# Kernel tuning notes

Measured on AMD Instinct MI355X. Metric: run time of the kernel, lower is better.

Reference implementation:

```python
import jax, jax.numpy as jnp
import numpy as np
from jax import lax

HID = 256
ITERS = 8
KT, KH, KW = 3, 7, 7
NBLK = 3
B_, T_, H_, W_, CIN = 1, 8, 32, 32, 128
NQ = 256


def _layernorm(x, scale, bias, eps=1e-6):
    mu = jnp.mean(x, axis=-1, keepdims=True)
    var = jnp.mean(jnp.square(x - mu), axis=-1, keepdims=True)
    return (x - mu) * lax.rsqrt(var + eps) * scale + bias


def _convssm3d(x, A_kernel, B_kernel):
    # x: (B,T,H,W,C); kernels: (C,kt,kh,kw)
    B, T, H, W, C = x.shape
    A_stable = 0.9 * jnp.tanh(A_kernel)
    tt = (jnp.arange(KT) - KT // 2) % T
    th = (jnp.arange(KH) - KH // 2) % H
    tw = (jnp.arange(KW) - KW // 2) % W
    TT, TH, TW = jnp.meshgrid(tt, th, tw, indexing='ij')

    def to_freq(k):
        pad = jnp.zeros((C, T, H, W), x.dtype).at[:, TT, TH, TW].set(k)
        return jnp.fft.fftn(pad, axes=(1, 2, 3)).transpose(1, 2, 3, 0)[None]  # (1,T,H,W,C)

    A_f = to_freq(A_stable)
    B_f = to_freq(B_kernel)
    Bx_f = B_f * jnp.fft.fftn(x, axes=(1, 2, 3))
    shape = (ITERS,) + x.shape
    a_seq = jnp.broadcast_to(A_f, shape)
    b_seq = jnp.broadcast_to(Bx_f, shape)

    def op(left, right):
        return (left[0] * right[0], right[0] * left[1] + right[1])

    _, h_all = lax.associative_scan(op, (a_seq, b_seq), axis=0)
    return jnp.fft.ifftn(h_all[-1], axes=(1, 2, 3)).real


def setup_inputs() -> dict:
    key = jax.random.key(0)
    ks = jax.random.split(key, 10)
    s = 0.02
    return {
        'video_features': jax.random.normal(ks[0], (B_, T_, H_, W_, CIN), jnp.float32),
        'query_points': jax.random.uniform(ks[1], (B_, NQ, 3), jnp.float32),
        'conv_w': jax.random.normal(ks[2], (CIN, HID), jnp.float32) * s,
        'conv_b': jnp.zeros((HID,), jnp.float32),
        'A_kernels': jax.random.normal(ks[3], (NBLK, HID, KT, KH, KW), jnp.float32) * s,
        'B_kernels': jax.random.normal(ks[4], (NBLK, HID, KT, KH, KW), jnp.float32) * s,
        'ln_scale': jnp.ones((NBLK, HID), jnp.float32),
        'ln_bias': jnp.zeros((NBLK, HID), jnp.float32),
        'mlp_w1': jax.random.normal(ks[5], (NBLK, HID, 4 * HID), jnp.float32) * s,
        'mlp_b1': jnp.zeros((NBLK, 4 * HID), jnp.float32),
        'mlp_w2': jax.random.normal(ks[6], (NBLK, 4 * HID, HID), jnp.float32) * s,
        'mlp_b2': jnp.zeros((NBLK, HID), jnp.float32),
        'traj_w': jax.random.normal(ks[7], (HID, 2), jnp.float32) * s,
        'traj_b': jnp.zeros((2,), jnp.float32),
        'occ_w': jax.random.normal(ks[8], (HID, 1), jnp.float32) * s,
        'occ_b': jnp.zeros((1,), jnp.float32),
    }


def reference(video_features, query_points, conv_w, conv_b, A_kernels, B_kernels,
              ln_scale, ln_bias, mlp_w1, mlp_b1, mlp_w2, mlp_b2,
              traj_w, traj_b, occ_w, occ_b):
    # 1x1x1 conv == channel dense. Query scatter in original is a zeros no-op.
    x = jnp.einsum('bthwc,cd->bthwd', video_features, conv_w) + conv_b
    for i in range(NBLK):
        h = _convssm3d(x, A_kernels[i], B_kernels[i])
        h = _layernorm(h, ln_scale[i], ln_bias[i])
        x = x + h
        m = jax.nn.gelu(x @ mlp_w1[i] + mlp_b1[i])  # approximate gelu (flax default)
        x = x + (m @ mlp_w2[i] + mlp_b2[i])
    feat = jnp.mean(x, axis=(2, 3))  # (B,T,C)
    N = query_points.shape[1]
    fe = jnp.broadcast_to(feat[:, None], (feat.shape[0], N) + feat.shape[1:])  # (B,N,T,C)
    trajectories = fe @ traj_w + traj_b + query_points[..., 1:3][:, :, None, :]  # (B,N,T,2)
    occlusion = jax.nn.sigmoid((fe @ occ_w + occ_b)[..., 0])  # (B,N,T)
    return trajectories, occlusion
```

## Files before the change

### kernel.cpp

```cpp
#include <hip/hip_runtime.h>
#include <hip/hip_bf16.h>
#include <math.h>

#define Tn 8
#define Hn 32
#define Wn 32
#define Pn 8192
#define Cn 256
#define CINn 128
#define NTAP 147
#define PADW 40

typedef short s8v __attribute__((ext_vector_type(8)));
typedef float f4v __attribute__((ext_vector_type(4)));
typedef __hip_bfloat16 bf16;

__device__ __forceinline__ float gelu_f(float v) {
    return 0.5f * v * (1.0f + tanhf(0.7978845608028654f * (v + 0.044715f * v * v * v)));
}

__device__ __forceinline__ void gload_lds16(const bf16* g, bf16* l) {
    __builtin_amdgcn_global_load_lds(
        (const __attribute__((address_space(1))) void*)g,
        (__attribute__((address_space(3))) void*)l, 16, 0, 0);
}

__device__ __forceinline__ size_t caddrA(int K, int m, int k) {
    return ((size_t)(m >> 7) * (K >> 6) + (k >> 6)) * 8192 +
           (size_t)((((k >> 3) & 7) * 128 + (m & 127)) * 8 + (k & 7));
}
__device__ __forceinline__ size_t caddrB(int K, int BN, int n, int k) {
    return ((size_t)(n / BN) * (K >> 6) + (k >> 6)) * (size_t)(BN * 64) +
           (size_t)((((k >> 3) & 7) * BN + (n % BN)) * 8 + (k & 7));
}

__global__ __launch_bounds__(256) void tcast_all_k(
        const float* __restrict__ convw, const float* __restrict__ w1,
        const float* __restrict__ w2, const float* __restrict__ video,
        bf16* __restrict__ cwT, bf16* __restrict__ w1T, bf16* __restrict__ w2T,
        bf16* __restrict__ vb) {
    const int z = blockIdx.z;
    const int tid = (int)threadIdx.x;
    if (z == 7) {
        const int bx = (int)blockIdx.y * 32 + (int)blockIdx.x;
        const int i = bx * 256 + tid;
        const int p = i >> 5, c0 = (i & 31) * 4;
        const float4 v = ((const float4*)video)[i];
        const size_t a0 = caddrA(CINn, p, c0);
        vb[a0 + 0] = __float2bfloat16(v.x);
        vb[a0 + 1] = __float2bfloat16(v.y);
        vb[a0 + 2] = __float2bfloat16(v.z);
        vb[a0 + 3] = __float2bfloat16(v.w);
        return;
    }
    const float* in;
    bf16* out;
    int R, C, bn;
    if (z == 0)      { in = convw;                       out = cwT;                          R = CINn; C = Cn;   bn = 32; }
    else if (z < 4)  { const int i = z - 1;
                       in = w1 + (size_t)i * Cn * 1024;  out = w1T + (size_t)i * 1024 * Cn;  R = Cn;   C = 1024; bn = 64; }
    else             { const int i = z - 4;
                       in = w2 + (size_t)i * 1024 * Cn;  out = w2T + (size_t)i * Cn * 1024;  R = 1024; C = Cn;   bn = 32; }
    if ((int)blockIdx.x >= (C >> 5) || (int)blockIdx.y >= (R >> 5)) return;

    __shared__ float tile[32][33];
    const int tx = tid & 31, ty = tid >> 5;
    const int rb = blockIdx.y << 5, cb = blockIdx.x << 5;
#pragma unroll
    for (int p = 0; p < 4; ++p)
        tile[ty + p * 8][tx] = in[(size_t)(rb + ty + p * 8) * C + cb + tx];
    __syncthreads();
#pragma unroll
    for (int p = 0; p < 4; ++p)
        out[caddrB(R, bn, cb + ty + p * 8, rb + tx)] = __float2bfloat16(tile[tx][ty + p * 8]);
}

template <int BN, int MODE, int ACH>
__global__ __launch_bounds__(256) void gemm_bf16_k(
        const bf16* __restrict__ A, const bf16* __restrict__ Wt,
        const float* __restrict__ bias, float* __restrict__ Cf,
        bf16* __restrict__ Cb, bf16* __restrict__ Cpl, int M, int N, int K) {
    constexpr int BM = 128;
    constexpr int NW = BN / 2;
    constexpr int NF = BN / 32;
    constexpr int ALOADS = 4;
    constexpr int BLOADS = (BN * 8) / 256;
    __shared__ s8v As[8 * BM];
    __shared__ s8v Bs[8 * BN];

    const int tid = (int)threadIdx.x;
    const int lane = tid & 63, wid = tid >> 6;
    const int wm = wid & 1, wn = wid >> 1;
    const int l15 = lane & 15, l4 = lane >> 4;
    const int m0 = blockIdx.y * BM;
    const int n0 = blockIdx.x * BN;

    f4v acc[4][NF];
#pragma unroll
    for (int i = 0; i < 4; ++i)
#pragma unroll
        for (int j = 0; j < NF; ++j)
#pragma unroll
            for (int r = 0; r < 4; ++r) acc[i][j][r] = 0.f;

    const bf16* Ach = A + ((size_t)(m0 >> 7) * (K >> 6)) * 8192;
    const bf16* Aln[ALOADS];
    if (ACH == 0) {
#pragma unroll
        for (int j = 0; j < ALOADS; ++j) {
            const int cid = j * 256 + tid;
            Aln[j] = A + (size_t)(m0 + (cid & (BM - 1))) * K + (cid / BM) * 8;
        }
    }
    const bf16* Bch = Wt + ((size_t)(n0 / BN) * (K >> 6)) * (size_t)(BN * 64);

    int kc = 0;
    for (int kb = 0; kb < K; kb += 64, ++kc) {
        if (ACH == 1) {
#pragma unroll
            for (int j = 0; j < ALOADS; ++j)
                gload_lds16(Ach + (size_t)kc * 8192 + (j * 256 + tid) * 8,
                            (bf16*)&As[j * 256 + tid]);
        } else {
#pragma unroll
            for (int j = 0; j < ALOADS; ++j)
                gload_lds16(Aln[j] + kb, (bf16*)&As[j * 256 + tid]);
        }
#pragma unroll
        for (int j = 0; j < BLOADS; ++j)
            gload_lds16(Bch + (size_t)kc * (BN * 64) + (j * 256 + tid) * 8,
                        (bf16*)&Bs[j * 256 + tid]);
        __syncthreads();

        s8v af[2][4], bfr[2][NF];
#pragma unroll
        for (int ks = 0; ks < 2; ++ks) {
#pragma unroll
            for (int i = 0; i < 4; ++i)
                af[ks][i] = As[(ks * 4 + l4) * BM + wm * 64 + i * 16 + l15];
#pragma unroll
            for (int j = 0; j < NF; ++j)
                bfr[ks][j] = Bs[(ks * 4 + l4) * BN + wn * NW + j * 16 + l15];
        }
#pragma unroll
        for (int ks = 0; ks < 2; ++ks)
#pragma unroll
            for (int i = 0; i < 4; ++i)
#pragma unroll
                for (int j = 0; j < NF; ++j)
                    acc[i][j] = __builtin_amdgcn_mfma_f32_16x16x32_bf16(
                        af[ks][i], bfr[ks][j], acc[i][j], 0, 0, 0);
        __syncthreads();
    }

#pragma unroll
    for (int i = 0; i < 4; ++i) {
        const int rbase = m0 + wm * 64 + i * 16 + l4 * 4;
#pragma unroll
        for (int j = 0; j < NF; ++j) {
            const int col = n0 + wn * NW + j * 16 + l15;
            const float bv = bias[col];
#pragma unroll
            for (int r = 0; r < 4; ++r) {
                const size_t idx = (size_t)(rbase + r) * N + col;
                float v = acc[i][j][r] + bv;
                if (MODE == 0) Cf[idx] = v;
                if (MODE == 1) Cb[caddrA(N, rbase + r, col)] = __float2bfloat16(gelu_f(v));
                if (MODE == 2) { v += Cf[idx]; Cf[idx] = v; }
                if (MODE != 1 && Cpl != nullptr)
                    Cpl[(size_t)col * Pn + rbase + r] = __float2bfloat16(v);
            }
        }
    }
}

#define CLOADS(AS, BS0, BS1, body) do {                                       \
    const int bb_ = (body);                                                   \
    const int kt_ = bb_ < 7 ? 0 : (bb_ < 14 ? 1 : 2);                         \
    const int kh_ = bb_ - kt_ * 7;                                            \
    BS0 = *(const s8v*)&tw[bb_][u0][0];                                       \
    BS1 = *(const s8v*)&tw[bb_][u1][0];                                       \
    _Pragma("unroll")                                                         \
    for (int i_ = 0; i_ < 2; ++i_) {                                          \
        const int tp_ = (tout[i_] - kt_ + 9) & 7;                             \
        const int hin_ = (hl[i_] + 35 - kh_) & 31;                            \
        AS[i_] = *(const s8v*)&pl[(tp_ * 32 + hin_) * PADW + aoff];           \
    }                                                                         \
} while (0)

#define CMFMA(AS, BS0, BS1) do {                                              \
    _Pragma("unroll")                                                         \
    for (int i_ = 0; i_ < 2; ++i_) {                                          \
        acc[i_][0] = __builtin_amdgcn_mfma_f32_16x16x32_bf16(AS[i_], BS0, acc[i_][0], 0, 0, 0); \
        acc[i_][1] = __builtin_amdgcn_mfma_f32_16x16x32_bf16(AS[i_], BS1, acc[i_][1], 0, 0, 0); \
    }                                                                         \
} while (0)

__global__ __launch_bounds__(512) void conv_ssm_k(
        const bf16* __restrict__ xplb,
        const float* __restrict__ Ak,
        const float* __restrict__ Bk,
        float* __restrict__ hpo) {
    __shared__ __align__(16) bf16 Pl[2][256 * PADW];
    __shared__ __align__(16) bf16 Tw[2][21][32][8];
    __shared__ float wtap[2][NTAP];

    const int c = blockIdx.x;
    const int tid = (int)threadIdx.x;
    const int lane = tid & 63, wv = tid >> 6;
    const int l15 = lane & 15, l4 = lane >> 4;

    if (tid < NTAP) {
        wtap[0][tid] = Bk[(size_t)c * NTAP + tid];
        wtap[1][tid] = 0.9f * tanhf(Ak[(size_t)c * NTAP + tid]);
    }
    {
        const s8v* src = (const s8v*)(xplb + (size_t)c * Pn);
#pragma unroll
        for (int j = 0; j < 2; ++j) {
            const int g = j * 512 + tid;
            *(s8v*)&Pl[0][(g >> 2) * PADW + (g & 3) * 8] = src[g];
        }
    }
    __syncthreads();
    for (int e = tid; e < 2 * 21 * 32; e += 512) {
        const int sel = e / 672, rem = e % 672;
        const int body = rem >> 5, u = rem & 31;
        const float* tp = &wtap[sel][body * 7];
        bf16 row[8];
#pragma unroll
        for (int j = 0; j < 8; ++j) {
            const int kw = (u - j) & 31;
            row[j] = __float2bfloat16((kw < 7) ? tp[kw] : 0.f);
        }
        *(s8v*)&Tw[sel][body][u][0] = *(const s8v*)row;
    }

    const int u0 = (l15 - l4 * 8 + 3) & 31;
    const int u1 = (l15 + 16 - l4 * 8 + 3) & 31;
    int tout[2], hl[2];
#pragma unroll
    for (int i = 0; i < 2; ++i) {
        const int f = wv * 2 + i;
        tout[i] = f >> 1;
        hl[i] = ((f & 1) << 4) + l15;
    }
    const int aoff = l4 * 8;

    float hsum[16];
#pragma unroll
    for (int i = 0; i < 16; ++i) hsum[i] = 0.f;
    __syncthreads();

#pragma unroll 1
    for (int it = 0; it < 8; ++it) {
        const bf16* pl = Pl[it & 1];
        bf16* pd = Pl[(it + 1) & 1];
        const bf16 (*tw)[32][8] = Tw[(it == 0) ? 0 : 1];

        f4v acc[2][2];
#pragma unroll
        for (int i = 0; i < 2; ++i)
#pragma unroll
            for (int hf = 0; hf < 2; ++hf)
#pragma unroll
                for (int r = 0; r < 4; ++r) acc[i][hf][r] = 0.f;

        s8v a0[2], a1[2], b00, b01, b10, b11;
        CLOADS(a0, b00, b01, 0);
#pragma unroll 1
        for (int b = 0; b < 20; b += 2) {
            CLOADS(a1, b10, b11, b + 1);
            CMFMA(a0, b00, b01);
            CLOADS(a0, b00, b01, b + 2);
            CMFMA(a1, b10, b11);
        }
        CMFMA(a0, b00, b01);

#pragma unroll
        for (int i = 0; i < 2; ++i) {
            const int rbase = (wv * 2 + i) * 16 + l4 * 4;
#pragma unroll
            for (int hf = 0; hf < 2; ++hf) {
                const int col = l15 + hf * 16;
#pragma unroll
                for (int r = 0; r < 4; ++r) {
                    const float v = acc[i][hf][r];
                    hsum[i * 8 + hf * 4 + r] += v;
                    if (it < 7) pd[(rbase + r) * PADW + col] = __float2bfloat16(v);
                }
            }
        }
        __syncthreads();
    }

    float* o = hpo + (size_t)c * Pn;
#pragma unroll
    for (int i = 0; i < 2; ++i) {
        const int rbase = (wv * 2 + i) * 16 + l4 * 4;
#pragma unroll
        for (int hf = 0; hf < 2; ++hf)
#pragma unroll
            for (int r = 0; r < 4; ++r)
                o[(rbase + r) * 32 + l15 + hf * 16] = hsum[i * 8 + hf * 4 + r];
    }
}

__global__ __launch_bounds__(256) void ln_res_plane_k(
        const float* __restrict__ hpl,
        const float* __restrict__ scale, const float* __restrict__ bias,
        float* __restrict__ x,
        bf16* __restrict__ xb) {
    __shared__ float tile[256][33];
    __shared__ float red[2][32][9];
    __shared__ float mus[32], rss[32];
    const int tid = (int)threadIdx.x;
    const int p0 = blockIdx.x << 5;

    {
        const float* src = hpl + (size_t)tid * Pn + p0;
#pragma unroll
        for (int j = 0; j < 32; j += 4) {
            const float4 v = *(const float4*)(src + j);
            tile[tid][j] = v.x; tile[tid][j + 1] = v.y;
            tile[tid][j + 2] = v.z; tile[tid][j + 3] = v.w;
        }
    }
    __syncthreads();
    {
        const int p = tid & 31, g = tid >> 5;
        float s = 0.f, ss = 0.f;
#pragma unroll
        for (int ci = 0; ci < 32; ++ci) {
            const float v = tile[g * 32 + ci][p];
            s += v; ss += v * v;
        }
        red[0][p][g] = s; red[1][p][g] = ss;
    }
    __syncthreads();
    if (tid < 32) {
        float s = 0.f, ss = 0.f;
#pragma unroll
        for (int g = 0; g < 8; ++g) { s += red[0][tid][g]; ss += red[1][tid][g]; }
        const float mu = s * (1.0f / 256.0f);
        const float var = ss * (1.0f / 256.0f) - mu * mu;
        mus[tid] = mu;
        rss[tid] = rsqrtf(var + 1e-6f);
    }
    __syncthreads();
    {
        const int cch = tid;
        const float sc = scale[cch], bi = bias[cch];
#pragma unroll 4
        for (int j = 0; j < 32; ++j) {
            const size_t idx = (size_t)(p0 + j) * Cn + cch;
            const float normed = (tile[cch][j] - mus[j]) * rss[j] * sc + bi;
            const float xv = x[idx] + normed;
            x[idx] = xv;
            xb[idx] = __float2bfloat16(xv);
        }
    }
}

__global__ void feat_part_k(const float* __restrict__ x, float* __restrict__ part) {
    const int t = blockIdx.x, sgm = blockIdx.y;
    const int c = (int)threadIdx.x;
    float acc = 0.f;
    const float* xp_ = x + ((size_t)t * 1024 + sgm * 128) * Cn + c;
    for (int p = 0; p < 128; ++p) acc += xp_[(size_t)p * Cn];
    part[(t * 8 + sgm) * Cn + c] = acc;
}

__global__ __launch_bounds__(256) void heads_k(
        const float* __restrict__ part, const float* __restrict__ qp,
        const float* __restrict__ traj_w, const float* __restrict__ traj_b,
        const float* __restrict__ occ_w, const float* __restrict__ occ_b,
        float* __restrict__ out) {
    __shared__ float fs[Tn * Cn];
    __shared__ float proj[Tn][3];
    const int tid = (int)threadIdx.x;
    for (int i = tid; i < Tn * Cn; i += 256) {
        const int t = i >> 8, c = i & 255;
        float s = 0.f;
#pragma unroll
        for (int j = 0; j < 8; ++j) s += part[(t * 8 + j) * Cn + c];
        fs[i] = s * (1.0f / 1024.0f);
    }
    __syncthreads();
    if (tid < 24) {
        const int t = tid / 3, j = tid % 3;
        float s = 0.f;
        for (int c = 0; c < Cn; ++c) {
            const float w = (j < 2) ? traj_w[c * 2 + j] : occ_w[c];
            s += fs[t * Cn + c] * w;
        }
        s += (j < 2) ? traj_b[j] : occ_b[0];
        proj[t][j] = s;
    }
    __syncthreads();
    const int n = tid;
#pragma unroll
    for (int t = 0; t < Tn; ++t) {
        out[(n * Tn + t) * 2 + 0] = proj[t][0] + qp[n * 3 + 1];
        out[(n * Tn + t) * 2 + 1] = proj[t][1] + qp[n * 3 + 2];
        out[4096 + n * Tn + t] = 1.0f / (1.0f + expf(-proj[t][2]));
    }
}

extern "C" void kernel_launch(void* const* d_in, const int* in_sizes, int n_in,
                              void* d_out, int out_size, void* d_ws, size_t ws_size,
                              hipStream_t stream) {
    const float* video = (const float*)d_in[0];
    const float* qp    = (const float*)d_in[1];
    const float* convw = (const float*)d_in[2];
    const float* convb = (const float*)d_in[3];
    const float* Ak    = (const float*)d_in[4];
    const float* Bk    = (const float*)d_in[5];
    const float* ln_s  = (const float*)d_in[6];
    const float* ln_b  = (const float*)d_in[7];
    const float* w1    = (const float*)d_in[8];
    const float* b1    = (const float*)d_in[9];
    const float* w2    = (const float*)d_in[10];
    const float* b2    = (const float*)d_in[11];
    const float* tw    = (const float*)d_in[12];
    const float* tb    = (const float*)d_in[13];
    const float* ow    = (const float*)d_in[14];
    const float* ob    = (const float*)d_in[15];

    char* wsb = (char*)d_ws;
    float* x    = (float*)wsb;           wsb += (size_t)Pn * Cn * 4;
    float* hpl  = (float*)wsb;           wsb += (size_t)Pn * Cn * 4;
    bf16*  xplb = (bf16*)wsb;            wsb += (size_t)Pn * Cn * 2;
    bf16*  xb   = (bf16*)wsb;            wsb += (size_t)Pn * Cn * 2;
    bf16*  mb   = (bf16*)wsb;            wsb += (size_t)Pn * 1024 * 2;
    bf16*  vb   = (bf16*)wsb;            wsb += (size_t)Pn * CINn * 2;
    bf16*  cwT  = (bf16*)wsb;            wsb += (size_t)Cn * CINn * 2;
    bf16*  w1T  = (bf16*)wsb;            wsb += (size_t)3 * 1024 * Cn * 2;
    bf16*  w2T  = (bf16*)wsb;            wsb += (size_t)3 * Cn * 1024 * 2;
    float* part = (float*)wsb;           wsb += (size_t)64 * Cn * 4;

    tcast_all_k<<<dim3(32, 32, 8), 256, 0, stream>>>(convw, w1, w2, video,
                                                     cwT, w1T, w2T, vb);

    gemm_bf16_k<32, 0, 1><<<dim3(Cn / 32, Pn / 128), 256, 0, stream>>>(
        vb, cwT, convb, x, nullptr, xplb, Pn, Cn, CINn);

    for (int i = 0; i < 3; ++i) {
        conv_ssm_k<<<Cn, 512, 0, stream>>>(xplb, Ak + (size_t)i * Cn * NTAP,
                                           Bk + (size_t)i * Cn * NTAP, hpl);
        ln_res_plane_k<<<Pn / 32, 256, 0, stream>>>(hpl, ln_s + i * Cn,
                                                    ln_b + i * Cn, x, xb);
        gemm_bf16_k<64, 1, 0><<<dim3(1024 / 64, Pn / 128), 256, 0, stream>>>(
            xb, w1T + (size_t)i * 1024 * Cn, b1 + (size_t)i * 1024, nullptr, mb,
            nullptr, Pn, 1024, Cn);
        gemm_bf16_k<32, 2, 1><<<dim3(Cn / 32, Pn / 128), 256, 0, stream>>>(
            mb, w2T + (size_t)i * Cn * 1024, b2 + (size_t)i * Cn, x, nullptr,
            (i < 2) ? xplb : nullptr, Pn, Cn, 1024);
    }

    feat_part_k<<<dim3(Tn, 8), 256, 0, stream>>>(x, part);
    heads_k<<<1, 256, 0, stream>>>(part, qp, tw, tb, ow, ob, (float*)d_out);
}
```

Measured before the change: 293.8 us.

## Double GEMM K-step per barrier and store SSM output in bf16

The GEMM kernel now loads two 64-wide K chunks into doubled LDS buffers before each barrier pair, which halves the number of __syncthreads per K loop. Separately, the conv-SSM output plane is written as bf16 instead of fp32, and the layernorm kernel reads bf16 and converts it back to float. This halves that intermediate's memory traffic. The cost is twice the LDS per GEMM block, which may lower occupancy, and bf16 rounding of the SSM output before layernorm.

```diff
diff --git a/kernel.cpp b/kernel.cpp
--- a/kernel.cpp
+++ b/kernel.cpp
@@ -17,6 +17,9 @@
 
 __device__ __forceinline__ float gelu_f(float v) {
     return 0.5f * v * (1.0f + tanhf(0.7978845608028654f * (v + 0.044715f * v * v * v)));
+}
+__device__ __forceinline__ float bf2f(short s) {
+    return __uint_as_float(((unsigned)(unsigned short)s) << 16);
 }
 
 __device__ __forceinline__ void gload_lds16(const bf16* g, bf16* l) {
@@ -83,10 +86,9 @@
     constexpr int BM = 128;
     constexpr int NW = BN / 2;
     constexpr int NF = BN / 32;
-    constexpr int ALOADS = 4;
     constexpr int BLOADS = (BN * 8) / 256;
-    __shared__ s8v As[8 * BM];
-    __shared__ s8v Bs[8 * BN];
+    __shared__ s8v As[16 * BM];
+    __shared__ s8v Bs[16 * BN];
 
     const int tid = (int)threadIdx.x;
     const int lane = tid & 63, wid = tid >> 6;
@@ -104,52 +106,55 @@
             for (int r = 0; r < 4; ++r) acc[i][j][r] = 0.f;
 
     const bf16* Ach = A + ((size_t)(m0 >> 7) * (K >> 6)) * 8192;
-    const bf16* Aln[ALOADS];
+    const bf16* Aln[4];
     if (ACH == 0) {
 #pragma unroll
-        for (int j = 0; j < ALOADS; ++j) {
+        for (int j = 0; j < 4; ++j) {
             const int cid = j * 256 + tid;
             Aln[j] = A + (size_t)(m0 + (cid & (BM - 1))) * K + (cid / BM) * 8;
         }
     }
     const bf16* Bch = Wt + ((size_t)(n0 / BN) * (K >> 6)) * (size_t)(BN * 64);
 
-    int kc = 0;
-    for (int kb = 0; kb < K; kb += 64, ++kc) {
-        if (ACH == 1) {
-#pragma unroll
-            for (int j = 0; j < ALOADS; ++j)
-                gload_lds16(Ach + (size_t)kc * 8192 + (j * 256 + tid) * 8,
-                            (bf16*)&As[j * 256 + tid]);
-        } else {
-#pragma unroll
-            for (int j = 0; j < ALOADS; ++j)
-                gload_lds16(Aln[j] + kb, (bf16*)&As[j * 256 + tid]);
-        }
-#pragma unroll
-        for (int j = 0; j < BLOADS; ++j)
-            gload_lds16(Bch + (size_t)kc * (BN * 64) + (j * 256 + tid) * 8,
-                        (bf16*)&Bs[j * 256 + tid]);
+    for (int kb = 0; kb < K; kb += 128) {
+        const int kc = kb >> 6;
+#pragma unroll
+        for (int u = 0; u < 2; ++u) {
+            if (ACH == 1) {
+#pragma unroll
+                for (int j = 0; j < 4; ++j)
+                    gload_lds16(Ach + (size_t)(kc + u) * 8192 + (j * 256 + tid) * 8,
+                                (bf16*)&As[u * 1024 + j * 256 + tid]);
+            } else {
+#pragma unroll
+                for (int j = 0; j < 4; ++j)
+                    gload_lds16(Aln[j] + kb + u * 64,
+                                (bf16*)&As[u * 1024 + j * 256 + tid]);
+            }
+#pragma unroll
+            for (int j = 0; j < BLOADS; ++j)
+                gload_lds16(Bch + (size_t)(kc + u) * (BN * 64) + (j * 256 + tid) * 8,
+                            (bf16*)&Bs[u * (8 * BN) + j * 256 + tid]);
+        }
         __syncthreads();
 
-        s8v af[2][4], bfr[2][NF];
-#pragma unroll
-        for (int ks = 0; ks < 2; ++ks) {
+#pragma unroll
+        for (int ksl = 0; ksl < 4; ++ksl) {
+            const int u = ksl >> 1, ks = ksl & 1;
+            s8v af[4], bfr[NF];
 #pragma unroll
             for (int i = 0; i < 4; ++i)
-                af[ks][i] = As[(ks * 4 + l4) * BM + wm * 64 + i * 16 + l15];
+                af[i] = As[u * 1024 + (ks * 4 + l4) * BM + wm * 64 + i * 16 + l15];
 #pragma unroll
             for (int j = 0; j < NF; ++j)
-                bfr[ks][j] = Bs[(ks * 4 + l4) * BN + wn * NW + j * 16 + l15];
-        }
-#pragma unroll
-        for (int ks = 0; ks < 2; ++ks)
+                bfr[j] = Bs[u * (8 * BN) + (ks * 4 + l4) * BN + wn * NW + j * 16 + l15];
 #pragma unroll
             for (int i = 0; i < 4; ++i)
 #pragma unroll
                 for (int j = 0; j < NF; ++j)
                     acc[i][j] = __builtin_amdgcn_mfma_f32_16x16x32_bf16(
-                        af[ks][i], bfr[ks][j], acc[i][j], 0, 0, 0);
+                        af[i], bfr[j], acc[i][j], 0, 0, 0);
+        }
         __syncthreads();
     }
 
@@ -200,7 +205,7 @@
         const bf16* __restrict__ xplb,
         const float* __restrict__ Ak,
         const float* __restrict__ Bk,
-        float* __restrict__ hpo) {
+        bf16* __restrict__ hpo) {
     __shared__ __align__(16) bf16 Pl[2][256 * PADW];
     __shared__ __align__(16) bf16 Tw[2][21][32][8];
     __shared__ float wtap[2][NTAP];
@@ -294,7 +299,7 @@
         __syncthreads();
     }
 
-    float* o = hpo + (size_t)c * Pn;
+    bf16* o = hpo + (size_t)c * Pn;
 #pragma unroll
     for (int i = 0; i < 2; ++i) {
         const int rbase = (wv * 2 + i) * 16 + l4 * 4;
@@ -302,12 +307,12 @@
         for (int hf = 0; hf < 2; ++hf)
 #pragma unroll
             for (int r = 0; r < 4; ++r)
-                o[(rbase + r) * 32 + l15 + hf * 16] = hsum[i * 8 + hf * 4 + r];
+                o[(rbase + r) * 32 + l15 + hf * 16] = __float2bfloat16(hsum[i * 8 + hf * 4 + r]);
     }
 }
 
 __global__ __launch_bounds__(256) void ln_res_plane_k(
-        const float* __restrict__ hpl,
+        const bf16* __restrict__ hpl,
         const float* __restrict__ scale, const float* __restrict__ bias,
         float* __restrict__ x,
         bf16* __restrict__ xb) {
@@ -318,12 +323,12 @@
     const int p0 = blockIdx.x << 5;
 
     {
-        const float* src = hpl + (size_t)tid * Pn + p0;
-#pragma unroll
-        for (int j = 0; j < 32; j += 4) {
-            const float4 v = *(const float4*)(src + j);
-            tile[tid][j] = v.x; tile[tid][j + 1] = v.y;
-            tile[tid][j + 2] = v.z; tile[tid][j + 3] = v.w;
+        const bf16* src = hpl + (size_t)tid * Pn + p0;
+#pragma unroll
+        for (int j = 0; j < 32; j += 8) {
+            const s8v v = *(const s8v*)(src + j);
+#pragma unroll
+            for (int e = 0; e < 8; ++e) tile[tid][j + e] = bf2f(v[e]);
         }
     }
     __syncthreads();
@@ -429,7 +434,7 @@
 
     char* wsb = (char*)d_ws;
     float* x    = (float*)wsb;           wsb += (size_t)Pn * Cn * 4;
-    float* hpl  = (float*)wsb;           wsb += (size_t)Pn * Cn * 4;
+    bf16*  hpl  = (bf16*)wsb;            wsb += (size_t)Pn * Cn * 2;
     bf16*  xplb = (bf16*)wsb;            wsb += (size_t)Pn * Cn * 2;
     bf16*  xb   = (bf16*)wsb;            wsb += (size_t)Pn * Cn * 2;
     bf16*  mb   = (bf16*)wsb;            wsb += (size_t)Pn * 1024 * 2;
```

Result: no change. 296.2 us (+0.8%).
